# Optimization experiments

Hardware: AMD Instinct MI355X
Metric: run time of the kernel (lower is better)

The kernel has to match this reference:

```python
import jax, jax.numpy as jnp
import numpy as np
import math

D_MODEL = 512
NUM_HEADS = 8
B, S = 2, 4096


def setup_inputs() -> dict:
    key = jax.random.key(0)
    ks = jax.random.split(key, 11)
    d = D_MODEL
    sc = 1.0 / math.sqrt(d)
    return {
        "query": jax.random.normal(ks[0], (B, S, d), jnp.float32),
        "key": jax.random.normal(ks[1], (B, S, d), jnp.float32),
        "value": jax.random.normal(ks[2], (B, S, d), jnp.float32),
        "Wq": jax.random.normal(ks[3], (d, d), jnp.float32) * sc,
        "bq": jnp.zeros((d,), jnp.float32),
        "Wk": jax.random.normal(ks[4], (d, d), jnp.float32) * sc,
        "bk": jnp.zeros((d,), jnp.float32),
        "Wv": jax.random.normal(ks[5], (d, d), jnp.float32) * sc,
        "bv": jnp.zeros((d,), jnp.float32),
        "Wo": jax.random.normal(ks[6], (d, d), jnp.float32) * sc,
        "bo": jnp.zeros((d,), jnp.float32),
    }


def reference(query, key, value, Wq, bq, Wk, bk, Wv, bv, Wo, bo):
    b, q_len, d_model = query.shape
    k_len = key.shape[1]
    h = NUM_HEADS
    d_k = d_model // h
    q = (query @ Wq.T + bq).reshape(b, q_len, h, d_k)
    k = (key @ Wk.T + bk).reshape(b, k_len, h, d_k)
    v = (value @ Wv.T + bv).reshape(b, k_len, h, d_k)
    # NOTE: faithful to source — softmax WITHOUT pre-scaling, then divide by sqrt(d_k)
    comp = jnp.einsum('bqhd,bkhd->bhqk', q, k)
    attn = jax.nn.softmax(comp, axis=-1) / jnp.sqrt(jnp.asarray(d_k, comp.dtype))
    x = jnp.einsum('bhqk,bkhd->bqhd', attn, v)
    return x.reshape(b, q_len, d_model) @ Wo.T + bo
```

## Files before the change

### kernel.cpp

```cpp
#include <hip/hip_runtime.h>

typedef _Float16 f16;
typedef __fp16 fp16x2 __attribute__((ext_vector_type(2)));
typedef _Float16 half4 __attribute__((ext_vector_type(4)));
typedef _Float16 half8 __attribute__((ext_vector_type(8)));
typedef float f32x4 __attribute__((ext_vector_type(4)));
typedef float float4v __attribute__((ext_vector_type(4)));
typedef float float2v __attribute__((ext_vector_type(2)));

#define LOG2E 1.44269504088896340736f

union H8 { fp16x2 h2[4]; half8 h8; };
union HV { half8 h8; half4 h4[2]; };

__device__ __forceinline__ float rowmax16(const f32x4 sf[4]) {
    float a = fmaxf(fmaxf(sf[0][0], sf[0][1]), fmaxf(sf[0][2], sf[0][3]));
    float b = fmaxf(fmaxf(sf[1][0], sf[1][1]), fmaxf(sf[1][2], sf[1][3]));
    float c = fmaxf(fmaxf(sf[2][0], sf[2][1]), fmaxf(sf[2][2], sf[2][3]));
    float d = fmaxf(fmaxf(sf[3][0], sf[3][1]), fmaxf(sf[3][2], sf[3][3]));
    return fmaxf(fmaxf(a, b), fmaxf(c, d));
}

__device__ __forceinline__ void max_defer(
    const f32x4 sf[4], float& mL, f32x4 o[4], f32x4& la)
{
    float vm = rowmax16(sf);
    vm = fmaxf(vm, __shfl_xor(vm, 16, 64));
    vm = fmaxf(vm, __shfl_xor(vm, 32, 64));
    float vmL = vm * LOG2E;
    if (__any(vmL > mL + 8.0f)) {
        float mn = fmaxf(mL, vmL);
        float al = __builtin_amdgcn_exp2f(mL - mn);
        la *= al;
        #pragma unroll
        for (int db = 0; db < 4; ++db) o[db] *= al;
        mL = mn;
    }
}

__device__ __forceinline__ void exp_pack(
    const f32x4 sf[4], float mL, H8& pb0, H8& pb1)
{
    float pe[16];
    #pragma unroll
    for (int kb = 0; kb < 4; ++kb)
        #pragma unroll
        for (int ro = 0; ro < 4; ++ro)
            pe[kb * 4 + ro] = __builtin_amdgcn_exp2f(fmaf(sf[kb][ro], LOG2E, -mL));
    pb0.h2[0] = __builtin_amdgcn_cvt_pkrtz(pe[0],  pe[1]);
    pb0.h2[1] = __builtin_amdgcn_cvt_pkrtz(pe[2],  pe[3]);
    pb0.h2[2] = __builtin_amdgcn_cvt_pkrtz(pe[4],  pe[5]);
    pb0.h2[3] = __builtin_amdgcn_cvt_pkrtz(pe[6],  pe[7]);
    pb1.h2[0] = __builtin_amdgcn_cvt_pkrtz(pe[8],  pe[9]);
    pb1.h2[1] = __builtin_amdgcn_cvt_pkrtz(pe[10], pe[11]);
    pb1.h2[2] = __builtin_amdgcn_cvt_pkrtz(pe[12], pe[13]);
    pb1.h2[3] = __builtin_amdgcn_cvt_pkrtz(pe[14], pe[15]);
}

__global__ __launch_bounds__(256) void qkv_proj(
    const float* __restrict__ Aq, const float* __restrict__ Ak, const float* __restrict__ Av,
    const float* __restrict__ Wq, const float* __restrict__ Wk, const float* __restrict__ Wv,
    const float* __restrict__ bq, const float* __restrict__ bk, const float* __restrict__ bv,
    f16* __restrict__ Qh, f16* __restrict__ Kh, f16* __restrict__ Vt)
{
    const int z = blockIdx.z;
    const float* __restrict__ A    = (z == 0) ? Aq : (z == 1) ? Ak : Av;
    const float* __restrict__ W    = (z == 0) ? Wq : (z == 1) ? Wk : Wv;
    const float* __restrict__ bias = (z == 0) ? bq : (z == 1) ? bk : bv;
    f16* __restrict__ dst          = (z == 0) ? Qh : (z == 1) ? Kh : Vt;

    __shared__ __align__(16) f16 As[128 * 40];
    __shared__ __align__(16) f16 Ws[128 * 40];

    const int t  = threadIdx.x;
    const int m0 = blockIdx.y * 128;
    const int n0 = blockIdx.x * 128;
    const int w = t >> 6, lane = t & 63, lr = lane & 15, lg = lane >> 4;
    const int wr = w >> 1, wc = w & 1;

    f32x4 acc[4][4] = {};

    for (int k0 = 0; k0 < 512; k0 += 32) {
        #pragma unroll
        for (int it = 0; it < 2; ++it) {
            int c = t + it * 256;
            int row  = c >> 2;
            int col8 = (c & 3) * 8;

            const float* ga = A + (size_t)(m0 + row) * 512 + k0 + col8;
            float4v a0 = *(const float4v*)ga;
            float4v a1 = *(const float4v*)(ga + 4);
            half8 ha;
            ha[0] = (f16)a0[0]; ha[1] = (f16)a0[1]; ha[2] = (f16)a0[2]; ha[3] = (f16)a0[3];
            ha[4] = (f16)a1[0]; ha[5] = (f16)a1[1]; ha[6] = (f16)a1[2]; ha[7] = (f16)a1[3];
            *(half8*)&As[row * 40 + col8] = ha;

            const float* gw = W + (size_t)(n0 + row) * 512 + k0 + col8;
            float4v w0 = *(const float4v*)gw;
            float4v w1 = *(const float4v*)(gw + 4);
            half8 hw;
            hw[0] = (f16)w0[0]; hw[1] = (f16)w0[1]; hw[2] = (f16)w0[2]; hw[3] = (f16)w0[3];
            hw[4] = (f16)w1[0]; hw[5] = (f16)w1[1]; hw[6] = (f16)w1[2]; hw[7] = (f16)w1[3];
            *(half8*)&Ws[row * 40 + col8] = hw;
        }
        __syncthreads();

        half8 af[4], bf[4];
        #pragma unroll
        for (int i = 0; i < 4; ++i) {
            af[i] = *(const half8*)&As[(wr * 64 + i * 16 + lr) * 40 + lg * 8];
            bf[i] = *(const half8*)&Ws[(wc * 64 + i * 16 + lr) * 40 + lg * 8];
        }
        #pragma unroll
        for (int mi = 0; mi < 4; ++mi)
            #pragma unroll
            for (int ni = 0; ni < 4; ++ni)
                acc[mi][ni] = __builtin_amdgcn_mfma_f32_16x16x32_f16(af[mi], bf[ni], acc[mi][ni], 0, 0, 0);
        __syncthreads();
    }

    if (z == 2) {
        #pragma unroll
        for (int mi = 0; mi < 4; ++mi) {
            #pragma unroll
            for (int ni = 0; ni < 4; ++ni) {
                int col = n0 + wc * 64 + ni * 16 + lr;
                float bv_ = bias[col];
                int h  = col >> 6;
                int dd = col & 63;
                int row0 = m0 + wr * 64 + mi * 16 + lg * 4;
                int b  = row0 >> 12;
                int s0 = row0 & 4095;
                half4 hv;
                hv[0] = (f16)(acc[mi][ni][0] + bv_);
                hv[1] = (f16)(acc[mi][ni][1] + bv_);
                hv[2] = (f16)(acc[mi][ni][2] + bv_);
                hv[3] = (f16)(acc[mi][ni][3] + bv_);
                *(half4*)&dst[(((size_t)(b * 8 + h)) * 64 + dd) * 4096 + s0] = hv;
            }
        }
    } else {
        #pragma unroll
        for (int mi = 0; mi < 4; ++mi) {
            #pragma unroll
            for (int ni = 0; ni < 4; ++ni) {
                int col = n0 + wc * 64 + ni * 16 + lr;
                float bv_ = bias[col];
                int h  = col >> 6;
                int dd = col & 63;
                #pragma unroll
                for (int r = 0; r < 4; ++r) {
                    int row = m0 + wr * 64 + mi * 16 + lg * 4 + r;
                    int b = row >> 12;
                    int s = row & 4095;
                    dst[(((size_t)(b * 8 + h)) * 4096 + s) * 64 + dd] = (f16)(acc[mi][ni][r] + bv_);
                }
            }
        }
    }
}

__global__ __launch_bounds__(256, 2) void flash_attn(
    const f16* __restrict__ Qh, const f16* __restrict__ Kh, const f16* __restrict__ Vt,
    f16* __restrict__ Xp, float2v* __restrict__ mlp)
{
    const int bh  = blockIdx.y;
    const int z   = blockIdx.z;
    const int t = threadIdx.x, w = t >> 6, lane = t & 63, lr = lane & 15, lg = lane >> 4;
    const int q0 = blockIdx.x * 128 + w * 32;

    __shared__ __align__(16) f16 Ks[2][64 * 72];
    __shared__ __align__(16) f16 Vs[2][64 * 72];

    const size_t hb = (size_t)bh * (4096 * 64);

    half8 aq00 = *(const half8*)&Qh[hb + (size_t)(q0 + lr) * 64 + lg * 8];
    half8 aq01 = *(const half8*)&Qh[hb + (size_t)(q0 + lr) * 64 + 32 + lg * 8];
    half8 aq10 = *(const half8*)&Qh[hb + (size_t)(q0 + 16 + lr) * 64 + lg * 8];
    half8 aq11 = *(const half8*)&Qh[hb + (size_t)(q0 + 16 + lr) * 64 + 32 + lg * 8];

    half8 ones;
    #pragma unroll
    for (int j = 0; j < 8; ++j) ones[j] = (f16)1.0f;
    const f32x4 zf = {0.0f, 0.0f, 0.0f, 0.0f};

    const int srow = t >> 3;
    const int u    = t & 7;
    const int scol = u * 8;
    const int kdstA = srow * 72 + scol;
    const int kdstB = kdstA + 32 * 72;
    const int vposb = ((u >> 2) & 1) * 32 + (u & 1) * 16 + ((u >> 1) & 1) * 4;
    const int vdstA = srow * 72 + vposb;
    const int vdstB = vdstA + 32 * 72;

    f32x4 o0[4] = {}, o1[4] = {};
    f32x4 la0 = {}, la1 = {};
    float mL0 = -INFINITY, mL1 = -INFINITY;

    const f16* kbase = Kh + hb + (size_t)(z * 2048 + srow) * 64 + scol;
    const f16* vbase = Vt + hb + (size_t)srow * 4096 + z * 2048 + scol;

    half8 kregA = *(const half8*)kbase;
    half8 kregB = *(const half8*)(kbase + 2048);
    half8 vregA = *(const half8*)vbase;
    half8 vregB = *(const half8*)(vbase + (size_t)32 * 4096);

    for (int kt = 0; kt < 2048; kt += 64) {
        const int bi = (kt >> 6) & 1;
        f16* ks = &Ks[bi][0];
        f16* vs = &Vs[bi][0];

        *(half8*)&ks[kdstA] = kregA;
        *(half8*)&ks[kdstB] = kregB;
        {
            HV a_; a_.h8 = vregA;
            *(half4*)&vs[vdstA]     = a_.h4[0];
            *(half4*)&vs[vdstA + 8] = a_.h4[1];
            HV b_; b_.h8 = vregB;
            *(half4*)&vs[vdstB]     = b_.h4[0];
            *(half4*)&vs[vdstB + 8] = b_.h4[1];
        }
        __syncthreads();

        int koff = ((kt + 64) & 2047);
        kregA = *(const half8*)(kbase + (size_t)koff * 64);
        kregB = *(const half8*)(kbase + 2048 + (size_t)koff * 64);
        vregA = *(const half8*)(vbase + koff);
        vregB = *(const half8*)(vbase + (size_t)32 * 4096 + koff);

        f32x4 sf0[4], sf1[4];
        {
            half8 kf[4];
            #pragma unroll
            for (int kb = 0; kb < 4; ++kb)
                kf[kb] = *(const half8*)&ks[(kb * 16 + lr) * 72 + lg * 8];
            __builtin_amdgcn_s_setprio(1);
            #pragma unroll
            for (int kb = 0; kb < 4; ++kb)
                sf0[kb] = __builtin_amdgcn_mfma_f32_16x16x32_f16(kf[kb], aq00, zf, 0, 0, 0);
            #pragma unroll
            for (int kb = 0; kb < 4; ++kb)
                sf1[kb] = __builtin_amdgcn_mfma_f32_16x16x32_f16(kf[kb], aq10, zf, 0, 0, 0);
            __builtin_amdgcn_s_setprio(0);
            #pragma unroll
            for (int kb = 0; kb < 4; ++kb)
                kf[kb] = *(const half8*)&ks[(kb * 16 + lr) * 72 + 32 + lg * 8];
            __builtin_amdgcn_s_setprio(1);
            #pragma unroll
            for (int kb = 0; kb < 4; ++kb)
                sf0[kb] = __builtin_amdgcn_mfma_f32_16x16x32_f16(kf[kb], aq01, sf0[kb], 0, 0, 0);
            #pragma unroll
            for (int kb = 0; kb < 4; ++kb)
                sf1[kb] = __builtin_amdgcn_mfma_f32_16x16x32_f16(kf[kb], aq11, sf1[kb], 0, 0, 0);
            __builtin_amdgcn_s_setprio(0);
        }

        max_defer(sf0, mL0, o0, la0);
        max_defer(sf1, mL1, o1, la1);

        half8 va[4], vb_[4];
        #pragma unroll
        for (int db = 0; db < 4; ++db) {
            va[db]  = *(const half8*)&vs[(db * 16 + lr) * 72 + lg * 8];
            vb_[db] = *(const half8*)&vs[(db * 16 + lr) * 72 + 32 + lg * 8];
        }

        H8 p00, p01, p10, p11;
        exp_pack(sf0, mL0, p00, p01);
        exp_pack(sf1, mL1, p10, p11);

        __builtin_amdgcn_s_setprio(1);
        o0[0] = __builtin_amdgcn_mfma_f32_16x16x32_f16(va[0], p00.h8, o0[0], 0, 0, 0);
        o0[1] = __builtin_amdgcn_mfma_f32_16x16x32_f16(va[1], p00.h8, o0[1], 0, 0, 0);
        o0[2] = __builtin_amdgcn_mfma_f32_16x16x32_f16(va[2], p00.h8, o0[2], 0, 0, 0);
        o0[3] = __builtin_amdgcn_mfma_f32_16x16x32_f16(va[3], p00.h8, o0[3], 0, 0, 0);
        o1[0] = __builtin_amdgcn_mfma_f32_16x16x32_f16(va[0], p10.h8, o1[0], 0, 0, 0);
        o1[1] = __builtin_amdgcn_mfma_f32_16x16x32_f16(va[1], p10.h8, o1[1], 0, 0, 0);
        o1[2] = __builtin_amdgcn_mfma_f32_16x16x32_f16(va[2], p10.h8, o1[2], 0, 0, 0);
        o1[3] = __builtin_amdgcn_mfma_f32_16x16x32_f16(va[3], p10.h8, o1[3], 0, 0, 0);
        la0 = __builtin_amdgcn_mfma_f32_16x16x32_f16(ones, p00.h8, la0, 0, 0, 0);
        la1 = __builtin_amdgcn_mfma_f32_16x16x32_f16(ones, p10.h8, la1, 0, 0, 0);
        o0[0] = __builtin_amdgcn_mfma_f32_16x16x32_f16(vb_[0], p01.h8, o0[0], 0, 0, 0);
        o0[1] = __builtin_amdgcn_mfma_f32_16x16x32_f16(vb_[1], p01.h8, o0[1], 0, 0, 0);
        o0[2] = __builtin_amdgcn_mfma_f32_16x16x32_f16(vb_[2], p01.h8, o0[2], 0, 0, 0);
        o0[3] = __builtin_amdgcn_mfma_f32_16x16x32_f16(vb_[3], p01.h8, o0[3], 0, 0, 0);
        o1[0] = __builtin_amdgcn_mfma_f32_16x16x32_f16(vb_[0], p11.h8, o1[0], 0, 0, 0);
        o1[1] = __builtin_amdgcn_mfma_f32_16x16x32_f16(vb_[1], p11.h8, o1[1], 0, 0, 0);
        o1[2] = __builtin_amdgcn_mfma_f32_16x16x32_f16(vb_[2], p11.h8, o1[2], 0, 0, 0);
        o1[3] = __builtin_amdgcn_mfma_f32_16x16x32_f16(vb_[3], p11.h8, o1[3], 0, 0, 0);
        la0 = __builtin_amdgcn_mfma_f32_16x16x32_f16(ones, p01.h8, la0, 0, 0, 0);
        la1 = __builtin_amdgcn_mfma_f32_16x16x32_f16(ones, p11.h8, la1, 0, 0, 0);
        __builtin_amdgcn_s_setprio(0);
    }

    const int b = bh >> 3, h = bh & 7;
    f16* X = Xp + (size_t)z * (8192 * 512);
    const float inv0 = 1.0f / la0[0];
    const float inv1 = 1.0f / la1[0];
    const int q0_ = q0 + lr, q1_ = q0 + 16 + lr;
    #pragma unroll
    for (int db = 0; db < 4; ++db) {
        half4 hv0, hv1;
        hv0[0] = (f16)(o0[db][0] * inv0);
        hv0[1] = (f16)(o0[db][1] * inv0);
        hv0[2] = (f16)(o0[db][2] * inv0);
        hv0[3] = (f16)(o0[db][3] * inv0);
        *(half4*)&X[((size_t)(b * 4096 + q0_)) * 512 + h * 64 + db * 16 + lg * 4] = hv0;
        hv1[0] = (f16)(o1[db][0] * inv1);
        hv1[1] = (f16)(o1[db][1] * inv1);
        hv1[2] = (f16)(o1[db][2] * inv1);
        hv1[3] = (f16)(o1[db][3] * inv1);
        *(half4*)&X[((size_t)(b * 4096 + q1_)) * 512 + h * 64 + db * 16 + lg * 4] = hv1;
    }

    if (lane < 16) {
        float2v m0v; m0v[0] = mL0; m0v[1] = la0[0];
        float2v m1v; m1v[0] = mL1; m1v[1] = la1[0];
        mlp[(size_t)z * 65536 + bh * 4096 + q0_] = m0v;
        mlp[(size_t)z * 65536 + bh * 4096 + q1_] = m1v;
    }
}

__global__ __launch_bounds__(256) void out_proj(
    const f16* __restrict__ Xp, const float2v* __restrict__ mlp,
    const float* __restrict__ Wo, const float* __restrict__ bo,
    float* __restrict__ out)
{
    __shared__ __align__(16) f16 As[128 * 40];
    __shared__ __align__(16) f16 Ws[128 * 40];

    const int t  = threadIdx.x;
    const int m0 = blockIdx.y * 128;
    const int n0 = blockIdx.x * 128;
    const int w = t >> 6, lane = t & 63, lr = lane & 15, lg = lane >> 4;
    const int wr = w >> 1, wc = w & 1;

    f32x4 acc[4][4] = {};

    for (int k0 = 0; k0 < 512; k0 += 32) {
        #pragma unroll
        for (int it = 0; it < 2; ++it) {
            int c = t + it * 256;
            int row  = c >> 2;
            int col8 = (c & 3) * 8;
            int gcol = k0 + col8;
            int tok  = m0 + row;

            int bhq = ((tok >> 12) * 8 + (gcol >> 6)) * 4096 + (tok & 4095);
            float2v ml1 = mlp[bhq];
            float2v ml2 = mlp[65536 + bhq];
            float mm = fmaxf(ml1[0], ml2[0]);
            float a1 = __builtin_amdgcn_exp2f(ml1[0] - mm) * ml1[1];
            float a2 = __builtin_amdgcn_exp2f(ml2[0] - mm) * ml2[1];
            float inv = 1.0f / (8.0f * (a1 + a2));
            float w1 = a1 * inv, w2 = a2 * inv;

            const size_t xoff = (size_t)tok * 512 + gcol;
            half8 x1 = *(const half8*)&Xp[xoff];
            half8 x2 = *(const half8*)&Xp[(size_t)8192 * 512 + xoff];
            half8 hx;
            #pragma unroll
            for (int j = 0; j < 8; ++j)
                hx[j] = (f16)(w1 * (float)x1[j] + w2 * (float)x2[j]);
            *(half8*)&As[row * 40 + col8] = hx;

            const float* gw = Wo + (size_t)(n0 + row) * 512 + k0 + col8;
            float4v w0 = *(const float4v*)gw;
            float4v w1v = *(const float4v*)(gw + 4);
            half8 hw;
            hw[0] = (f16)w0[0];  hw[1] = (f16)w0[1];  hw[2] = (f16)w0[2];  hw[3] = (f16)w0[3];
            hw[4] = (f16)w1v[0]; hw[5] = (f16)w1v[1]; hw[6] = (f16)w1v[2]; hw[7] = (f16)w1v[3];
            *(half8*)&Ws[row * 40 + col8] = hw;
        }
        __syncthreads();

        half8 af[4], bf[4];
        #pragma unroll
        for (int i = 0; i < 4; ++i) {
            af[i] = *(const half8*)&As[(wr * 64 + i * 16 + lr) * 40 + lg * 8];
            bf[i] = *(const half8*)&Ws[(wc * 64 + i * 16 + lr) * 40 + lg * 8];
        }
        #pragma unroll
        for (int mi = 0; mi < 4; ++mi)
            #pragma unroll
            for (int ni = 0; ni < 4; ++ni)
                acc[mi][ni] = __builtin_amdgcn_mfma_f32_16x16x32_f16(af[mi], bf[ni], acc[mi][ni], 0, 0, 0);
        __syncthreads();
    }

    #pragma unroll
    for (int mi = 0; mi < 4; ++mi) {
        #pragma unroll
        for (int ni = 0; ni < 4; ++ni) {
            int col = n0 + wc * 64 + ni * 16 + lr;
            float bb = bo[col];
            #pragma unroll
            for (int r = 0; r < 4; ++r) {
                int row = m0 + wr * 64 + mi * 16 + lg * 4 + r;
                out[(size_t)row * 512 + col] = acc[mi][ni][r] + bb;
            }
        }
    }
}

extern "C" void kernel_launch(void* const* d_in, const int* in_sizes, int n_in,
                              void* d_out, int out_size, void* d_ws, size_t ws_size,
                              hipStream_t stream) {
    const float* query = (const float*)d_in[0];
    const float* key   = (const float*)d_in[1];
    const float* value = (const float*)d_in[2];
    const float* Wq    = (const float*)d_in[3];
    const float* bq    = (const float*)d_in[4];
    const float* Wk    = (const float*)d_in[5];
    const float* bk    = (const float*)d_in[6];
    const float* Wv    = (const float*)d_in[7];
    const float* bv    = (const float*)d_in[8];
    const float* Wo    = (const float*)d_in[9];
    const float* bo    = (const float*)d_in[10];
    float* out = (float*)d_out;

    char* ws = (char*)d_ws;
    f16*     Qh  = (f16*)(ws);
    f16*     Kh  = (f16*)(ws + 8388608);
    f16*     Vt  = (f16*)(ws + 16777216);
    f16*     Xp  = (f16*)(ws + 25165824);
    float2v* mlp = (float2v*)(ws + 41943040);

    qkv_proj<<<dim3(4, 64, 3), 256, 0, stream>>>(query, key, value,
                                                 Wq, Wk, Wv, bq, bk, bv,
                                                 Qh, Kh, Vt);
    flash_attn<<<dim3(32, 16, 2), 256, 0, stream>>>(Qh, Kh, Vt, Xp, mlp);
    out_proj<<<dim3(4, 64), 256, 0, stream>>>(Xp, mlp, Wo, bo, out);
}
```

Measured before the change: 170.4 us.

## Pre-convert weights to fp16 and split split-K combine into its own kernel

Adds a kernel that converts all four fp32 weight matrices to fp16 once per call, so the projection GEMMs load half-width weights with no in-loop conversion. Moves the merge of the two flash-attention key halves (softmax renormalization) out of out_proj into a separate combine kernel, written into the freed Q buffer. This cuts redundant weight conversion and mlp reads repeated across column blocks, at the cost of two extra launches and an extra round trip of the combined activation through memory.

```diff
diff --git a/kernel.cpp b/kernel.cpp
--- a/kernel.cpp
+++ b/kernel.cpp
@@ -57,15 +57,31 @@
     pb1.h2[3] = __builtin_amdgcn_cvt_pkrtz(pe[14], pe[15]);
 }
 
+__global__ __launch_bounds__(256) void wcvt(
+    const float* __restrict__ Wq, const float* __restrict__ Wk,
+    const float* __restrict__ Wv, const float* __restrict__ Wo,
+    f16* __restrict__ dst)
+{
+    const int m = blockIdx.y;
+    const float* __restrict__ src = (m == 0) ? Wq : (m == 1) ? Wk : (m == 2) ? Wv : Wo;
+    const size_t i = ((size_t)blockIdx.x * 256 + threadIdx.x) * 8;
+    float4v a0 = *(const float4v*)(src + i);
+    float4v a1 = *(const float4v*)(src + i + 4);
+    half8 h;
+    h[0] = (f16)a0[0]; h[1] = (f16)a0[1]; h[2] = (f16)a0[2]; h[3] = (f16)a0[3];
+    h[4] = (f16)a1[0]; h[5] = (f16)a1[1]; h[6] = (f16)a1[2]; h[7] = (f16)a1[3];
+    *(half8*)&dst[(size_t)m * 262144 + i] = h;
+}
+
 __global__ __launch_bounds__(256) void qkv_proj(
     const float* __restrict__ Aq, const float* __restrict__ Ak, const float* __restrict__ Av,
-    const float* __restrict__ Wq, const float* __restrict__ Wk, const float* __restrict__ Wv,
+    const f16* __restrict__ Wh,
     const float* __restrict__ bq, const float* __restrict__ bk, const float* __restrict__ bv,
     f16* __restrict__ Qh, f16* __restrict__ Kh, f16* __restrict__ Vt)
 {
     const int z = blockIdx.z;
     const float* __restrict__ A    = (z == 0) ? Aq : (z == 1) ? Ak : Av;
-    const float* __restrict__ W    = (z == 0) ? Wq : (z == 1) ? Wk : Wv;
+    const f16*   __restrict__ W    = Wh + (size_t)z * 262144;
     const float* __restrict__ bias = (z == 0) ? bq : (z == 1) ? bk : bv;
     f16* __restrict__ dst          = (z == 0) ? Qh : (z == 1) ? Kh : Vt;
 
@@ -95,13 +111,8 @@
             ha[4] = (f16)a1[0]; ha[5] = (f16)a1[1]; ha[6] = (f16)a1[2]; ha[7] = (f16)a1[3];
             *(half8*)&As[row * 40 + col8] = ha;
 
-            const float* gw = W + (size_t)(n0 + row) * 512 + k0 + col8;
-            float4v w0 = *(const float4v*)gw;
-            float4v w1 = *(const float4v*)(gw + 4);
-            half8 hw;
-            hw[0] = (f16)w0[0]; hw[1] = (f16)w0[1]; hw[2] = (f16)w0[2]; hw[3] = (f16)w0[3];
-            hw[4] = (f16)w1[0]; hw[5] = (f16)w1[1]; hw[6] = (f16)w1[2]; hw[7] = (f16)w1[3];
-            *(half8*)&Ws[row * 40 + col8] = hw;
+            *(half8*)&Ws[row * 40 + col8] =
+                *(const half8*)&W[(size_t)(n0 + row) * 512 + k0 + col8];
         }
         __syncthreads();
 
@@ -321,10 +332,37 @@
     }
 }
 
+__global__ __launch_bounds__(256) void combine_halves(
+    const f16* __restrict__ Xp, const float2v* __restrict__ mlp,
+    f16* __restrict__ Xh)
+{
+    const size_t idx  = (size_t)blockIdx.x * 256 + threadIdx.x;
+    const size_t flat = idx * 8;
+    const int h = (int)((flat >> 6) & 7);
+    const int s = (int)((flat >> 9) & 4095);
+    const int b = (int)(flat >> 21);
+    const int bhq = (b * 8 + h) * 4096 + s;
+
+    float2v ml1 = mlp[bhq];
+    float2v ml2 = mlp[65536 + bhq];
+    float mm = fmaxf(ml1[0], ml2[0]);
+    float a1 = __builtin_amdgcn_exp2f(ml1[0] - mm) * ml1[1];
+    float a2 = __builtin_amdgcn_exp2f(ml2[0] - mm) * ml2[1];
+    float inv = 1.0f / (8.0f * (a1 + a2));
+    float w1 = a1 * inv, w2 = a2 * inv;
+
+    half8 x1 = *(const half8*)&Xp[flat];
+    half8 x2 = *(const half8*)&Xp[(size_t)8192 * 512 + flat];
+    half8 r;
+    #pragma unroll
+    for (int j = 0; j < 8; ++j)
+        r[j] = (f16)(w1 * (float)x1[j] + w2 * (float)x2[j]);
+    *(half8*)&Xh[flat] = r;
+}
+
 __global__ __launch_bounds__(256) void out_proj(
-    const f16* __restrict__ Xp, const float2v* __restrict__ mlp,
-    const float* __restrict__ Wo, const float* __restrict__ bo,
-    float* __restrict__ out)
+    const f16* __restrict__ Xh, const f16* __restrict__ Woh,
+    const float* __restrict__ bo, float* __restrict__ out)
 {
     __shared__ __align__(16) f16 As[128 * 40];
     __shared__ __align__(16) f16 Ws[128 * 40];
@@ -343,34 +381,11 @@
             int c = t + it * 256;
             int row  = c >> 2;
             int col8 = (c & 3) * 8;
-            int gcol = k0 + col8;
-            int tok  = m0 + row;
-
-            int bhq = ((tok >> 12) * 8 + (gcol >> 6)) * 4096 + (tok & 4095);
-            float2v ml1 = mlp[bhq];
-            float2v ml2 = mlp[65536 + bhq];
-            float mm = fmaxf(ml1[0], ml2[0]);
-            float a1 = __builtin_amdgcn_exp2f(ml1[0] - mm) * ml1[1];
-            float a2 = __builtin_amdgcn_exp2f(ml2[0] - mm) * ml2[1];
-            float inv = 1.0f / (8.0f * (a1 + a2));
-            float w1 = a1 * inv, w2 = a2 * inv;
-
-            const size_t xoff = (size_t)tok * 512 + gcol;
-            half8 x1 = *(const half8*)&Xp[xoff];
-            half8 x2 = *(const half8*)&Xp[(size_t)8192 * 512 + xoff];
-            half8 hx;
-            #pragma unroll
-            for (int j = 0; j < 8; ++j)
-                hx[j] = (f16)(w1 * (float)x1[j] + w2 * (float)x2[j]);
-            *(half8*)&As[row * 40 + col8] = hx;
-
-            const float* gw = Wo + (size_t)(n0 + row) * 512 + k0 + col8;
-            float4v w0 = *(const float4v*)gw;
-            float4v w1v = *(const float4v*)(gw + 4);
-            half8 hw;
-            hw[0] = (f16)w0[0];  hw[1] = (f16)w0[1];  hw[2] = (f16)w0[2];  hw[3] = (f16)w0[3];
-            hw[4] = (f16)w1v[0]; hw[5] = (f16)w1v[1]; hw[6] = (f16)w1v[2]; hw[7] = (f16)w1v[3];
-            *(half8*)&Ws[row * 40 + col8] = hw;
+
+            *(half8*)&As[row * 40 + col8] =
+                *(const half8*)&Xh[(size_t)(m0 + row) * 512 + k0 + col8];
+            *(half8*)&Ws[row * 40 + col8] =
+                *(const half8*)&Woh[(size_t)(n0 + row) * 512 + k0 + col8];
         }
         __syncthreads();
 
@@ -425,10 +440,13 @@
     f16*     Vt  = (f16*)(ws + 16777216);
     f16*     Xp  = (f16*)(ws + 25165824);
     float2v* mlp = (float2v*)(ws + 41943040);
-
-    qkv_proj<<<dim3(4, 64, 3), 256, 0, stream>>>(query, key, value,
-                                                 Wq, Wk, Wv, bq, bk, bv,
-                                                 Qh, Kh, Vt);
+    f16*     Wh  = (f16*)(ws + 43008000);
+    f16*     Xh  = Qh;
+
+    wcvt<<<dim3(128, 4), 256, 0, stream>>>(Wq, Wk, Wv, Wo, Wh);
+    qkv_proj<<<dim3(4, 64, 3), 256, 0, stream>>>(query, key, value, Wh,
+                                                 bq, bk, bv, Qh, Kh, Vt);
     flash_attn<<<dim3(32, 16, 2), 256, 0, stream>>>(Qh, Kh, Vt, Xp, mlp);
-    out_proj<<<dim3(4, 64), 256, 0, stream>>>(Xp, mlp, Wo, bo, out);
-}
+    combine_halves<<<2048, 256, 0, stream>>>(Xp, mlp, Xh);
+    out_proj<<<dim3(4, 64), 256, 0, stream>>>(Xh, Wh + 3 * 262144, bo, out);
+}
```

Result: no change. 167.2 us (-1.8%).

## Split attention KV range three ways and add separate combine kernel

Applied to the files above, without the earlier changes.

The flash attention grid now splits the 4096 keys into three uneven chunks (22/21/21 tiles) instead of two, which gives more blocks for better CU occupancy. The LDS K/V buffers go from double to single buffering, with an extra barrier per tile. Merging the partial results moves out of out_proj into a new combine3 kernel that writes a merged f16 X into the Q buffer. This adds a kernel launch and an extra round trip through global memory for X, but makes the out_proj load path simpler.

```diff
diff --git a/kernel.cpp b/kernel.cpp
--- a/kernel.cpp
+++ b/kernel.cpp
@@ -169,8 +169,11 @@
     const int t = threadIdx.x, w = t >> 6, lane = t & 63, lr = lane & 15, lg = lane >> 4;
     const int q0 = blockIdx.x * 128 + w * 32;
 
-    __shared__ __align__(16) f16 Ks[2][64 * 72];
-    __shared__ __align__(16) f16 Vs[2][64 * 72];
+    const int nt  = (z == 0) ? 22 : 21;
+    const int kb0 = (z == 0) ? 0 : (22 + (z - 1) * 21) * 64;
+
+    __shared__ __align__(16) f16 Ks[64 * 72];
+    __shared__ __align__(16) f16 Vs[64 * 72];
 
     const size_t hb = (size_t)bh * (4096 * 64);
 
@@ -197,32 +200,29 @@
     f32x4 la0 = {}, la1 = {};
     float mL0 = -INFINITY, mL1 = -INFINITY;
 
-    const f16* kbase = Kh + hb + (size_t)(z * 2048 + srow) * 64 + scol;
-    const f16* vbase = Vt + hb + (size_t)srow * 4096 + z * 2048 + scol;
+    const f16* kbase = Kh + hb + (size_t)(kb0 + srow) * 64 + scol;
+    const f16* vbase = Vt + hb + (size_t)srow * 4096 + kb0 + scol;
 
     half8 kregA = *(const half8*)kbase;
     half8 kregB = *(const half8*)(kbase + 2048);
     half8 vregA = *(const half8*)vbase;
     half8 vregB = *(const half8*)(vbase + (size_t)32 * 4096);
 
-    for (int kt = 0; kt < 2048; kt += 64) {
-        const int bi = (kt >> 6) & 1;
-        f16* ks = &Ks[bi][0];
-        f16* vs = &Vs[bi][0];
-
-        *(half8*)&ks[kdstA] = kregA;
-        *(half8*)&ks[kdstB] = kregB;
+    for (int it = 0; it < nt; ++it) {
+        __syncthreads();
+        *(half8*)&Ks[kdstA] = kregA;
+        *(half8*)&Ks[kdstB] = kregB;
         {
             HV a_; a_.h8 = vregA;
-            *(half4*)&vs[vdstA]     = a_.h4[0];
-            *(half4*)&vs[vdstA + 8] = a_.h4[1];
+            *(half4*)&Vs[vdstA]     = a_.h4[0];
+            *(half4*)&Vs[vdstA + 8] = a_.h4[1];
             HV b_; b_.h8 = vregB;
-            *(half4*)&vs[vdstB]     = b_.h4[0];
-            *(half4*)&vs[vdstB + 8] = b_.h4[1];
-        }
-        __syncthreads();
-
-        int koff = ((kt + 64) & 2047);
+            *(half4*)&Vs[vdstB]     = b_.h4[0];
+            *(half4*)&Vs[vdstB + 8] = b_.h4[1];
+        }
+        __syncthreads();
+
+        int koff = ((it + 1 < nt) ? (it + 1) : 0) * 64;
         kregA = *(const half8*)(kbase + (size_t)koff * 64);
         kregB = *(const half8*)(kbase + 2048 + (size_t)koff * 64);
         vregA = *(const half8*)(vbase + koff);
@@ -233,7 +233,7 @@
             half8 kf[4];
             #pragma unroll
             for (int kb = 0; kb < 4; ++kb)
-                kf[kb] = *(const half8*)&ks[(kb * 16 + lr) * 72 + lg * 8];
+                kf[kb] = *(const half8*)&Ks[(kb * 16 + lr) * 72 + lg * 8];
             __builtin_amdgcn_s_setprio(1);
             #pragma unroll
             for (int kb = 0; kb < 4; ++kb)
@@ -244,7 +244,7 @@
             __builtin_amdgcn_s_setprio(0);
             #pragma unroll
             for (int kb = 0; kb < 4; ++kb)
-                kf[kb] = *(const half8*)&ks[(kb * 16 + lr) * 72 + 32 + lg * 8];
+                kf[kb] = *(const half8*)&Ks[(kb * 16 + lr) * 72 + 32 + lg * 8];
             __builtin_amdgcn_s_setprio(1);
             #pragma unroll
             for (int kb = 0; kb < 4; ++kb)
@@ -261,8 +261,8 @@
         half8 va[4], vb_[4];
         #pragma unroll
         for (int db = 0; db < 4; ++db) {
-            va[db]  = *(const half8*)&vs[(db * 16 + lr) * 72 + lg * 8];
-            vb_[db] = *(const half8*)&vs[(db * 16 + lr) * 72 + 32 + lg * 8];
+            va[db]  = *(const half8*)&Vs[(db * 16 + lr) * 72 + lg * 8];
+            vb_[db] = *(const half8*)&Vs[(db * 16 + lr) * 72 + 32 + lg * 8];
         }
 
         H8 p00, p01, p10, p11;
@@ -321,10 +321,40 @@
     }
 }
 
+__global__ __launch_bounds__(256) void combine3(
+    const f16* __restrict__ Xp, const float2v* __restrict__ mlp,
+    f16* __restrict__ Xh)
+{
+    const size_t idx  = (size_t)blockIdx.x * 256 + threadIdx.x;
+    const size_t flat = idx * 8;
+    const int h = (int)((flat >> 6) & 7);
+    const int s = (int)((flat >> 9) & 4095);
+    const int b = (int)(flat >> 21);
+    const int bhq = (b * 8 + h) * 4096 + s;
+
+    float2v ml0 = mlp[bhq];
+    float2v ml1 = mlp[65536 + bhq];
+    float2v ml2 = mlp[131072 + bhq];
+    float mm = fmaxf(fmaxf(ml0[0], ml1[0]), ml2[0]);
+    float a0 = __builtin_amdgcn_exp2f(ml0[0] - mm) * ml0[1];
+    float a1 = __builtin_amdgcn_exp2f(ml1[0] - mm) * ml1[1];
+    float a2 = __builtin_amdgcn_exp2f(ml2[0] - mm) * ml2[1];
+    float inv = 1.0f / (8.0f * (a0 + a1 + a2));
+    float w0 = a0 * inv, w1 = a1 * inv, w2 = a2 * inv;
+
+    half8 x0 = *(const half8*)&Xp[flat];
+    half8 x1 = *(const half8*)&Xp[(size_t)8192 * 512 + flat];
+    half8 x2 = *(const half8*)&Xp[(size_t)2 * 8192 * 512 + flat];
+    half8 r;
+    #pragma unroll
+    for (int j = 0; j < 8; ++j)
+        r[j] = (f16)(w0 * (float)x0[j] + w1 * (float)x1[j] + w2 * (float)x2[j]);
+    *(half8*)&Xh[flat] = r;
+}
+
 __global__ __launch_bounds__(256) void out_proj(
-    const f16* __restrict__ Xp, const float2v* __restrict__ mlp,
-    const float* __restrict__ Wo, const float* __restrict__ bo,
-    float* __restrict__ out)
+    const f16* __restrict__ Xh, const float* __restrict__ Wo,
+    const float* __restrict__ bo, float* __restrict__ out)
 {
     __shared__ __align__(16) f16 As[128 * 40];
     __shared__ __align__(16) f16 Ws[128 * 40];
@@ -343,33 +373,16 @@
             int c = t + it * 256;
             int row  = c >> 2;
             int col8 = (c & 3) * 8;
-            int gcol = k0 + col8;
-            int tok  = m0 + row;
-
-            int bhq = ((tok >> 12) * 8 + (gcol >> 6)) * 4096 + (tok & 4095);
-            float2v ml1 = mlp[bhq];
-            float2v ml2 = mlp[65536 + bhq];
-            float mm = fmaxf(ml1[0], ml2[0]);
-            float a1 = __builtin_amdgcn_exp2f(ml1[0] - mm) * ml1[1];
-            float a2 = __builtin_amdgcn_exp2f(ml2[0] - mm) * ml2[1];
-            float inv = 1.0f / (8.0f * (a1 + a2));
-            float w1 = a1 * inv, w2 = a2 * inv;
-
-            const size_t xoff = (size_t)tok * 512 + gcol;
-            half8 x1 = *(const half8*)&Xp[xoff];
-            half8 x2 = *(const half8*)&Xp[(size_t)8192 * 512 + xoff];
-            half8 hx;
-            #pragma unroll
-            for (int j = 0; j < 8; ++j)
-                hx[j] = (f16)(w1 * (float)x1[j] + w2 * (float)x2[j]);
-            *(half8*)&As[row * 40 + col8] = hx;
+
+            *(half8*)&As[row * 40 + col8] =
+                *(const half8*)&Xh[(size_t)(m0 + row) * 512 + k0 + col8];
 
             const float* gw = Wo + (size_t)(n0 + row) * 512 + k0 + col8;
             float4v w0 = *(const float4v*)gw;
-            float4v w1v = *(const float4v*)(gw + 4);
+            float4v w1 = *(const float4v*)(gw + 4);
             half8 hw;
-            hw[0] = (f16)w0[0];  hw[1] = (f16)w0[1];  hw[2] = (f16)w0[2];  hw[3] = (f16)w0[3];
-            hw[4] = (f16)w1v[0]; hw[5] = (f16)w1v[1]; hw[6] = (f16)w1v[2]; hw[7] = (f16)w1v[3];
+            hw[0] = (f16)w0[0]; hw[1] = (f16)w0[1]; hw[2] = (f16)w0[2]; hw[3] = (f16)w0[3];
+            hw[4] = (f16)w1[0]; hw[5] = (f16)w1[1]; hw[6] = (f16)w1[2]; hw[7] = (f16)w1[3];
             *(half8*)&Ws[row * 40 + col8] = hw;
         }
         __syncthreads();
@@ -424,11 +437,13 @@
     f16*     Kh  = (f16*)(ws + 8388608);
     f16*     Vt  = (f16*)(ws + 16777216);
     f16*     Xp  = (f16*)(ws + 25165824);
-    float2v* mlp = (float2v*)(ws + 41943040);
+    float2v* mlp = (float2v*)(ws + 50331648);
+    f16*     Xh  = Qh;
 
     qkv_proj<<<dim3(4, 64, 3), 256, 0, stream>>>(query, key, value,
                                                  Wq, Wk, Wv, bq, bk, bv,
                                                  Qh, Kh, Vt);
-    flash_attn<<<dim3(32, 16, 2), 256, 0, stream>>>(Qh, Kh, Vt, Xp, mlp);
-    out_proj<<<dim3(4, 64), 256, 0, stream>>>(Xp, mlp, Wo, bo, out);
-}
+    flash_attn<<<dim3(32, 16, 3), 256, 0, stream>>>(Qh, Kh, Vt, Xp, mlp);
+    combine3<<<2048, 256, 0, stream>>>(Xp, mlp, Xh);
+    out_proj<<<dim3(4, 64), 256, 0, stream>>>(Xh, Wo, bo, out);
+}
```

After: 165.7 us. 1.03x faster.
